# Optimization experiments

Measured on AMD Instinct MI355X. Metric: run time of the kernel, lower is better.

## Reference

```python
import jax, jax.numpy as jnp
import numpy as np
from jax import lax

DIM = 192
NUM_CLASSES = 4
D_INNER = 2 * DIM          # expand=2
D_STATE = 16
D_CONV = 4
DT_RANK = (DIM + 15) // 16  # ceil(192/16)=12
PATCH = 16


def _mamba_params(key, prefix):
    ks = jax.random.split(key, 9)
    s = lambda k, shape, scale: (jax.random.normal(k, shape, jnp.float32) * scale)
    p = {
        prefix + '_in_w':   s(ks[0], (2 * D_INNER, DIM), 0.02),
        prefix + '_conv_w': s(ks[1], (D_INNER, D_CONV), 0.1),
        prefix + '_conv_b': jnp.zeros((D_INNER,), jnp.float32),
        prefix + '_xproj_w': s(ks[2], (DT_RANK + 2 * D_STATE, D_INNER), 0.02),
        prefix + '_dt_w':   s(ks[3], (D_INNER, DT_RANK), 0.1),
        prefix + '_dt_b':   s(ks[4], (D_INNER,), 0.1),
        # A_log init: log(1..d_state) broadcast over d_inner (mamba default)
        prefix + '_A_log':  jnp.broadcast_to(jnp.log(jnp.arange(1, D_STATE + 1, dtype=jnp.float32)), (D_INNER, D_STATE)) + 0.0,
        prefix + '_D':      jnp.ones((D_INNER,), jnp.float32),
        prefix + '_out_w':  s(ks[5], (DIM, D_INNER), 0.02),
    }
    return p


def setup_inputs() -> dict:
    key = jax.random.key(0)
    ks = jax.random.split(key, 8)
    inp = {
        'x': jax.random.normal(ks[0], (32, 3, 384, 384), jnp.float32),
        'patch_w': jax.random.normal(ks[1], (DIM, 3, PATCH, PATCH), jnp.float32) * 0.02,
        'patch_b': jnp.zeros((DIM,), jnp.float32),
        'ln_g': jnp.ones((DIM,), jnp.float32),
        'ln_b': jnp.zeros((DIM,), jnp.float32),
        'fc_w': jax.random.normal(ks[2], (NUM_CLASSES, DIM), jnp.float32) * 0.02,
        'fc_b': jnp.zeros((NUM_CLASSES,), jnp.float32),
    }
    inp.update(_mamba_params(ks[3], 'f'))
    inp.update(_mamba_params(ks[4], 'b'))
    return inp


def _layernorm(x, g, b, eps=1e-5):
    mu = jnp.mean(x, -1, keepdims=True)
    var = jnp.mean(jnp.square(x - mu), -1, keepdims=True)
    return (x - mu) * lax.rsqrt(var + eps) * g + b


def _mamba(x, in_w, conv_w, conv_b, xproj_w, dt_w, dt_b, A_log, Dskip, out_w):
    # x: [B, L, DIM]
    Bn, L, _ = x.shape
    xz = x @ in_w.T                                    # [B, L, 2*di]
    xi, z = jnp.split(xz, 2, axis=-1)
    # causal depthwise conv1d, kernel D_CONV, left pad
    xp = jnp.pad(xi, ((0, 0), (D_CONV - 1, 0), (0, 0)))
    xc = conv_b + sum(xp[:, k:k + L, :] * conv_w[:, k] for k in range(D_CONV))
    xc = jax.nn.silu(xc)                               # [B, L, di]
    proj = xc @ xproj_w.T                              # [B, L, dtr+2*ds]
    dt, Bm, Cm = jnp.split(proj, [DT_RANK, DT_RANK + D_STATE], axis=-1)
    dt = jax.nn.softplus(dt @ dt_w.T + dt_b)           # [B, L, di]
    A = -jnp.exp(A_log)                                # [di, ds]

    def step(h, inp):
        dt_t, B_t, C_t, x_t = inp                      # [B,di],[B,ds],[B,ds],[B,di]
        dA = jnp.exp(dt_t[:, :, None] * A)             # [B, di, ds]
        h = dA * h + (dt_t * x_t)[:, :, None] * B_t[:, None, :]
        y = jnp.einsum('bds,bs->bd', h, C_t)
        return h, y

    h0 = jnp.zeros((Bn, D_INNER, D_STATE), x.dtype)
    xs = (dt.transpose(1, 0, 2), Bm.transpose(1, 0, 2),
          Cm.transpose(1, 0, 2), xc.transpose(1, 0, 2))
    _, ys = lax.scan(step, h0, xs)                     # [L, B, di]
    y = ys.transpose(1, 0, 2) + xc * Dskip
    y = y * jax.nn.silu(z)
    return y @ out_w.T                                 # [B, L, DIM]


def reference(x, patch_w, patch_b, ln_g, ln_b, fc_w, fc_b,
              f_in_w, f_conv_w, f_conv_b, f_xproj_w, f_dt_w, f_dt_b, f_A_log, f_D, f_out_w,
              b_in_w, b_conv_w, b_conv_b, b_xproj_w, b_dt_w, b_dt_b, b_A_log, b_D, b_out_w):
    Bn, C, H, W = x.shape
    Hp, Wp = H // PATCH, W // PATCH
    # patch embed: stride==kernel conv == reshape + einsum
    xr = x.reshape(Bn, C, Hp, PATCH, Wp, PATCH)
    tok = jnp.einsum('bchpwq,dcpq->bhwd', xr, patch_w) + patch_b
    tok = tok.reshape(Bn, Hp * Wp, DIM)                # [B, L, D]
    tok = _layernorm(tok, ln_g, ln_b)
    fwd = _mamba(tok, f_in_w, f_conv_w, f_conv_b, f_xproj_w, f_dt_w, f_dt_b, f_A_log, f_D, f_out_w)
    bwd = _mamba(tok[:, ::-1, :], b_in_w, b_conv_w, b_conv_b, b_xproj_w, b_dt_w, b_dt_b, b_A_log, b_D, b_out_w)
    out = fwd + bwd[:, ::-1, :]
    pooled = jnp.mean(out, axis=1)                     # adaptive avg pool to 1
    return pooled @ fc_w.T + fc_b                      # [B, num_classes]
```

## Files before the change

### kernel.cpp

```cpp
#include <hip/hip_runtime.h>
#include <hip/hip_bf16.h>

#define NC 32
#define CL 18

typedef __attribute__((ext_vector_type(8))) short short8;
typedef __attribute__((ext_vector_type(4))) float f32x4;
typedef __attribute__((ext_vector_type(2))) float f32x2;

__device__ __forceinline__ float sigm(float x){ return 1.0f/(1.0f+__expf(-x)); }

__device__ __forceinline__ ushort f2bf(float f){
  unsigned u = __float_as_uint(f);
  unsigned r = (u + 0x7fffu + ((u>>16)&1u)) >> 16;
  return (ushort)r;
}
__device__ __forceinline__ float bf2f(ushort h){ return __uint_as_float(((unsigned)h)<<16); }

__global__ __launch_bounds__(256) void k_prep_all(
    const float* __restrict__ patch_w, const float* __restrict__ f_in_w,
    const float* __restrict__ b_in_w,
    const float* __restrict__ f_xw, const float* __restrict__ b_xw,
    const float* __restrict__ f_cw, const float* __restrict__ b_cw,
    const float* __restrict__ f_al, const float* __restrict__ b_al,
    const float* __restrict__ fc_w, const float* __restrict__ f_ow,
    const float* __restrict__ b_ow,
    ushort* __restrict__ pw_h, ushort* __restrict__ pw_l,
    ushort* __restrict__ iw_h, ushort* __restrict__ iw_l,
    ushort* __restrict__ xw_h, ushort* __restrict__ xw_l,
    float* __restrict__ cwT, float* __restrict__ Abuf,
    float* __restrict__ A0fl, float* __restrict__ W2){
  const int bx = blockIdx.x, t = threadIdx.x;
  if (bx < 1728){
    int which = bx/576;
    int i = (bx - which*576)*256 + t;
    if (which==0){
      float f = patch_w[i];
      ushort hb = f2bf(f);
      pw_h[i]=hb; pw_l[i]=f2bf(f - bf2f(hb));
    } else {
      const float* src = (which==1) ? f_in_w : b_in_w;
      int dirofs = (which==1) ? 0 : 48;
      float f = src[i];
      int n = i/192, k = i%192;
      int nblk = n>>4, r = n&15, kblk = k>>5, kk = k&31;
      int lane = r + ((kk>>3)<<4), j = kk&7;
      size_t idx = ((size_t)((nblk+dirofs)*6 + kblk)*64 + lane)*8 + j;
      ushort hb = f2bf(f);
      iw_h[idx]=hb; iw_l[idx]=f2bf(f - bf2f(hb));
    }
  } else if (bx < 1872){
    int i = (bx-1728)*256 + t;
    int dir=i/(48*384), rem=i%(48*384), n=rem/384, k=rem%384;
    float v = (n<44) ? (dir?b_xw:f_xw)[n*384+k] : 0.f;
    ushort hb = f2bf(v);
    xw_h[i]=hb; xw_l[i]=f2bf(v - bf2f(hb));
  } else if (bx < 1884){
    int i = (bx-1872)*256 + t;
    int dir=i/1536, rem=i%1536, j=rem/384, k=rem%384;
    cwT[i] = (dir ? b_cw : f_cw)[k*4+j];
  } else if (bx < 1887){
    int i = (bx-1884)*256 + t;
    if (i < 768){
      int dir=i/384, di=i%384;
      const float* alp = (dir?b_al:f_al) + di*16;
      float A0 = -expf(alp[0]);
      bool fast = true;
      Abuf[(size_t)i*16] = A0;
      #pragma unroll
      for (int s=1;s<16;s++){
        float A = -expf(alp[s]);
        Abuf[(size_t)i*16+s] = A;
        fast = fast && (fabsf(A - (s+1)*A0) <= 1e-5f*(s+1)*fabsf(A0));
      }
      A0fl[i*2]=A0; A0fl[i*2+1]=fast?1.f:0.f;
    }
  } else {
    int i = (bx-1887)*256 + t;
    if (i < 768){
      int dir=i/384, di=i%384;
      const float* ow = dir ? b_ow : f_ow;
      float a0=0.f,a1=0.f,a2=0.f,a3=0.f;
      for (int d=0; d<192; ++d){
        float o = ow[d*384 + di];
        a0 += fc_w[0*192+d]*o; a1 += fc_w[1*192+d]*o;
        a2 += fc_w[2*192+d]*o; a3 += fc_w[3*192+d]*o;
      }
      W2[(0*2+dir)*384+di]=a0; W2[(1*2+dir)*384+di]=a1;
      W2[(2*2+dir)*384+di]=a2; W2[(3*2+dir)*384+di]=a3;
    }
  }
}

__global__ __launch_bounds__(1024) void k_patch(
    const float* __restrict__ x,
    const ushort* __restrict__ pw_h, const ushort* __restrict__ pw_l,
    const float* __restrict__ pb, const float* __restrict__ lng,
    const float* __restrict__ lnb,
    ushort* __restrict__ tokf_h, ushort* __restrict__ tokf_l,
    int b0, int Mc){
  __shared__ __align__(16) char sBmem[49152];
  __shared__ __align__(16) ushort sAh[64*64], sAl[64*64];
  __shared__ float sLN[4][64][2];
  ushort* sBh = (ushort*)sBmem;
  ushort* sBl = (ushort*)(sBmem + 24576);
  const int tid = threadIdx.x;
  const int m0 = blockIdx.x*64;
  const int lane = tid&63, w = tid>>6;
  const int wr = w>>2, wc = w&3;
  const int r = lane&15, g = lane>>4;
  f32x4 acc[3];
  #pragma unroll
  for (int i=0;i<3;i++) acc[i] = (f32x4){0.f,0.f,0.f,0.f};

  const int mA = tid>>4, remA = tid&15, ppA = remA>>2, qqA = remA&3;
  const int rmA = m0 + mA;
  const bool okA = (rmA < Mc);
  size_t baseA = 0;
  if (okA){
    int b = b0 + rmA/576, l = rmA%576, hp = l/24, wp = l%24;
    baseA = ((size_t)(b*3)*384 + hp*16 + ppA)*96 + wp*4 + qqA;
  }
  const int nB0 = tid>>3, k8B0 = tid&7;
  const bool okB1 = (tid < 512);
  const int fB1 = tid + 1024;
  const int nB1 = fB1>>3, k8B1 = fB1&7;
  const int byteA  = (mA*128 + ppA*32 + qqA*8) ^ ((mA&7)<<4);
  const int byteB0 = (nB0*128 + k8B0*16) ^ ((nB0&7)<<4);
  const int byteB1 = (nB1*128 + k8B1*16) ^ ((nB1&7)<<4);

  float4 vA = make_float4(0.f,0.f,0.f,0.f);
  uint4 vBh0 = {}, vBl0 = {}, vBh1 = {}, vBl1 = {};
  {
    if (okA) vA = reinterpret_cast<const float4*>(x)[baseA];
    size_t gi0 = (size_t)nB0*768 + k8B0*8;
    vBh0 = *reinterpret_cast<const uint4*>(pw_h + gi0);
    vBl0 = *reinterpret_cast<const uint4*>(pw_l + gi0);
    if (okB1){
      size_t gi1 = (size_t)nB1*768 + k8B1*8;
      vBh1 = *reinterpret_cast<const uint4*>(pw_h + gi1);
      vBl1 = *reinterpret_cast<const uint4*>(pw_l + gi1);
    }
  }

  for (int s=0;s<12;s++){
    {
      ushort4 hv, lv;
      hv.x=f2bf(vA.x); lv.x=f2bf(vA.x-bf2f(hv.x));
      hv.y=f2bf(vA.y); lv.y=f2bf(vA.y-bf2f(hv.y));
      hv.z=f2bf(vA.z); lv.z=f2bf(vA.z-bf2f(hv.z));
      hv.w=f2bf(vA.w); lv.w=f2bf(vA.w-bf2f(hv.w));
      *reinterpret_cast<ushort4*>((char*)sAh + byteA) = hv;
      *reinterpret_cast<ushort4*>((char*)sAl + byteA) = lv;
      *reinterpret_cast<uint4*>((char*)sBh + byteB0) = vBh0;
      *reinterpret_cast<uint4*>((char*)sBl + byteB0) = vBl0;
      if (okB1){
        *reinterpret_cast<uint4*>((char*)sBh + byteB1) = vBh1;
        *reinterpret_cast<uint4*>((char*)sBl + byteB1) = vBl1;
      }
    }
    __syncthreads();
    if (s < 11){
      int s1 = s+1, c1 = s1>>2, p01 = (s1&3)*4;
      if (okA) vA = reinterpret_cast<const float4*>(x)[baseA + ((size_t)c1*384 + p01)*96];
      size_t gi0 = (size_t)nB0*768 + (size_t)s1*64 + k8B0*8;
      vBh0 = *reinterpret_cast<const uint4*>(pw_h + gi0);
      vBl0 = *reinterpret_cast<const uint4*>(pw_l + gi0);
      if (okB1){
        size_t gi1 = (size_t)nB1*768 + (size_t)s1*64 + k8B1*8;
        vBh1 = *reinterpret_cast<const uint4*>(pw_h + gi1);
        vBl1 = *reinterpret_cast<const uint4*>(pw_l + gi1);
      }
    }
    #pragma unroll
    for (int kk=0;kk<2;kk++){
      int arow = wr*16 + r;
      int abyte = (arow*128 + kk*64 + g*16) ^ ((arow&7)<<4);
      short8 ah = *reinterpret_cast<const short8*>((char*)sAh + abyte);
      short8 al = *reinterpret_cast<const short8*>((char*)sAl + abyte);
      #pragma unroll
      for (int nfl=0; nfl<3; nfl++){
        int brow = (wc*3+nfl)*16 + r;
        int bbyte = (brow*128 + kk*64 + g*16) ^ ((brow&7)<<4);
        short8 bh = *reinterpret_cast<const short8*>((char*)sBh + bbyte);
        short8 bll = *reinterpret_cast<const short8*>((char*)sBl + bbyte);
        acc[nfl] = __builtin_amdgcn_mfma_f32_16x16x32_bf16(ah, bh, acc[nfl], 0,0,0);
        acc[nfl] = __builtin_amdgcn_mfma_f32_16x16x32_bf16(ah, bll, acc[nfl], 0,0,0);
        acc[nfl] = __builtin_amdgcn_mfma_f32_16x16x32_bf16(al, bh, acc[nfl], 0,0,0);
      }
    }
    __syncthreads();
  }
  float pbv[3], gv[3], bv[3];
  #pragma unroll
  for (int nfl=0;nfl<3;nfl++){
    int col = (wc*3+nfl)*16 + r;
    pbv[nfl]=pb[col]; gv[nfl]=lng[col]; bv[nfl]=lnb[col];
  }
  #pragma unroll
  for (int nfl=0;nfl<3;nfl++)
    #pragma unroll
    for (int q=0;q<4;q++) acc[nfl][q] += pbv[nfl];
  float sum[4]={0,0,0,0}, sq[4]={0,0,0,0};
  #pragma unroll
  for (int nfl=0;nfl<3;nfl++)
    #pragma unroll
    for (int q=0;q<4;q++){ float v=acc[nfl][q]; sum[q]+=v; sq[q]+=v*v; }
  #pragma unroll
  for (int off=1; off<16; off<<=1){
    #pragma unroll
    for (int q=0;q<4;q++){
      sum[q]+=__shfl_xor(sum[q],off);
      sq[q] +=__shfl_xor(sq[q],off);
    }
  }
  if (r==0){
    #pragma unroll
    for (int q=0;q<4;q++){
      int row = wr*16 + g*4 + q;
      sLN[wc][row][0]=sum[q]; sLN[wc][row][1]=sq[q];
    }
  }
  __syncthreads();
  float* sT = (float*)sBmem;
  #pragma unroll
  for (int q=0;q<4;q++){
    int rl = wr*16 + g*4 + q;
    float stot = sLN[0][rl][0]+sLN[1][rl][0]+sLN[2][rl][0]+sLN[3][rl][0];
    float qtot = sLN[0][rl][1]+sLN[1][rl][1]+sLN[2][rl][1]+sLN[3][rl][1];
    float mu = stot*(1.f/192.f);
    float var = qtot*(1.f/192.f) - mu*mu;
    float rs = rsqrtf(var + 1e-5f);
    #pragma unroll
    for (int nfl=0;nfl<3;nfl++)
      sT[rl*192 + (wc*3+nfl)*16 + r] = (acc[nfl][q]-mu)*rs*gv[nfl] + bv[nfl];
  }
  __syncthreads();
  const int mB = m0>>4;
  #pragma unroll
  for (int i=0;i<2;i++){
    int fl = tid + 1024*i;
    if (fl < 1536){
      int mb = fl/384, rem = fl-mb*384, kb = rem>>6, ln = rem&63;
      int rr = ln&15, gq = ln>>4;
      const float* sp = sT + (mb*16+rr)*192 + kb*32 + gq*8;
      short8 hv, lv;
      #pragma unroll
      for (int j=0;j<8;j++){
        float v = sp[j];
        ushort hb = f2bf(v);
        hv[j] = (short)hb;
        lv[j] = (short)f2bf(v - bf2f(hb));
      }
      size_t o = ((size_t)((mB+mb)*6 + kb)*64 + ln)*8;
      *reinterpret_cast<short8*>(tokf_h + o) = hv;
      *reinterpret_cast<short8*>(tokf_l + o) = lv;
    }
  }
}

__global__ __launch_bounds__(1024) void k_inproj(
    const ushort* __restrict__ tokf_h, const ushort* __restrict__ tokf_l,
    const ushort* __restrict__ iw_h, const ushort* __restrict__ iw_l,
    float* __restrict__ xib, ushort* __restrict__ zb, int Bc, int Mc){
  __shared__ __align__(16) char sMem[65536];
  ushort* sAh = (ushort*)sMem;
  ushort* sAl = (ushort*)(sMem + 16384);
  ushort* sBh = (ushort*)(sMem + 32768);
  ushort* sBl = (ushort*)(sMem + 49152);
  const int tid = threadIdx.x;
  const int lane = tid&63, w = tid>>6;
  const int wr = w>>2, wc = w&3;
  const int r = lane&15, g = lane>>4;
  const int m0 = blockIdx.x*128;
  const int mb0 = blockIdx.x*8;
  const int nb0 = blockIdx.y*8;
  const int n0d = (blockIdx.y%6)*128;
  const bool dir1 = (blockIdx.y >= 6);
  const bool isZ = ((blockIdx.y%6) >= 3);

  f32x4 acc[2][2];
  #pragma unroll
  for (int a=0;a<2;a++)
    #pragma unroll
    for (int b=0;b<2;b++) acc[a][b] = (f32x4){0.f,0.f,0.f,0.f};

  for (int s=0;s<3;s++){
    {
      const int f = w;
      const int mf = f>>1, kk = f&1;
      const size_t ga = ((size_t)((mb0+mf)*6 + 2*s+kk)*64 + lane)*8;
      const size_t gb = ((size_t)((nb0+mf)*6 + 2*s+kk)*64 + lane)*8;
      const int so = f*512 + lane*8;
      *reinterpret_cast<short8*>(sAh+so) = *reinterpret_cast<const short8*>(tokf_h+ga);
      *reinterpret_cast<short8*>(sBh+so) = *reinterpret_cast<const short8*>(iw_h+gb);
      if (!isZ){
        *reinterpret_cast<short8*>(sAl+so) = *reinterpret_cast<const short8*>(tokf_l+ga);
        *reinterpret_cast<short8*>(sBl+so) = *reinterpret_cast<const short8*>(iw_l+gb);
      }
    }
    __syncthreads();
    #pragma unroll
    for (int kk=0;kk<2;kk++){
      short8 ah[2], al[2];
      #pragma unroll
      for (int mf=0;mf<2;mf++){
        const int fo = ((wr*2+mf)*2+kk)*512 + lane*8;
        ah[mf] = *reinterpret_cast<const short8*>(sAh+fo);
        if (!isZ) al[mf] = *reinterpret_cast<const short8*>(sAl+fo);
      }
      #pragma unroll
      for (int nf=0;nf<2;nf++){
        const int fo = ((wc*2+nf)*2+kk)*512 + lane*8;
        short8 bh = *reinterpret_cast<const short8*>(sBh+fo);
        if (isZ){
          #pragma unroll
          for (int mf=0;mf<2;mf++)
            acc[mf][nf] = __builtin_amdgcn_mfma_f32_16x16x32_bf16(ah[mf], bh, acc[mf][nf], 0,0,0);
        } else {
          short8 bl = *reinterpret_cast<const short8*>(sBl+fo);
          #pragma unroll
          for (int mf=0;mf<2;mf++){
            acc[mf][nf] = __builtin_amdgcn_mfma_f32_16x16x32_bf16(ah[mf], bh, acc[mf][nf], 0,0,0);
            acc[mf][nf] = __builtin_amdgcn_mfma_f32_16x16x32_bf16(ah[mf], bl, acc[mf][nf], 0,0,0);
            acc[mf][nf] = __builtin_amdgcn_mfma_f32_16x16x32_bf16(al[mf], bh, acc[mf][nf], 0,0,0);
          }
        }
      }
    }
    __syncthreads();
  }

  float* sT = reinterpret_cast<float*>(sMem);
  const int h_of_w = wr>>1;
  #pragma unroll
  for (int h=0; h<2; h++){
    if (h==1) __syncthreads();
    if (h_of_w == h){
      #pragma unroll
      for (int mf=0;mf<2;mf++)
        #pragma unroll
        for (int nf=0;nf<2;nf++)
          #pragma unroll
          for (int q=0;q<4;q++){
            int rl = (wr&1)*32 + mf*16 + g*4 + q;
            int c  = wc*32 + nf*16 + r;
            sT[rl*132 + c] = acc[mf][nf][q];
          }
    }
    __syncthreads();
    {
      const int rl = tid>>4, cg = tid&15;
      const int rm = m0 + h*64 + rl;
      if (rm < Mc){
        size_t row;
        if (dir1){
          int bl = rm/576, l = rm - bl*576;
          row = (size_t)(Bc + bl)*576 + (575-l);
        } else {
          row = (size_t)rm;
        }
        const float* sp = sT + rl*132 + cg*8;
        if (!isZ){
          *reinterpret_cast<f32x4*>(xib + row*384 + n0d + cg*8)     = *reinterpret_cast<const f32x4*>(sp);
          *reinterpret_cast<f32x4*>(xib + row*384 + n0d + cg*8 + 4) = *reinterpret_cast<const f32x4*>(sp+4);
        } else {
          short8 hv;
          #pragma unroll
          for (int j=0;j<8;j++){
            float v = sp[j];
            v = v*sigm(v);
            hv[j] = (short)f2bf(v);
          }
          *reinterpret_cast<short8*>(zb + row*384 + (n0d-384) + cg*8) = hv;
        }
      }
    }
  }
}

__global__ __launch_bounds__(256) void k_convx(
    const float* __restrict__ xib, const float* __restrict__ cwT,
    const float* __restrict__ f_cb, const float* __restrict__ b_cb,
    const ushort* __restrict__ xw_h, const ushort* __restrict__ xw_l,
    float* __restrict__ proj, ushort* __restrict__ xcb, int Bc){
  __shared__ __align__(16) float sRaw[67*64];
  __shared__ __align__(16) ushort sAh[64*64], sAl[64*64];
  __shared__ __align__(16) ushort sBh[48*64], sBl[48*64];
  const int dir = blockIdx.z, blk = blockIdx.y, l0 = blockIdx.x*64;
  const int tid = threadIdx.x, lane = tid&63, w = tid>>6;
  const int r = lane&15, g = lane>>4;
  const size_t seq = ((size_t)dir*Bc + blk)*576;
  const float* cwTd = cwT + dir*1536;
  const float* cbp  = dir?b_cb:f_cb;
  const ushort* bhp = xw_h + dir*48*384;
  const ushort* blp = xw_l + dir*48*384;
  f32x4 acc[3];
  #pragma unroll
  for (int i=0;i<3;i++) acc[i] = (f32x4){0.f,0.f,0.f,0.f};

  for (int kc=0; kc<6; ++kc){
    #pragma unroll
    for (int i=0;i<5;i++){
      int f = tid + i*256;
      if (f < 67*16){
        int rr = f>>4, kq = f&15;
        int l = l0 + rr - 3;
        float4 v = make_float4(0.f,0.f,0.f,0.f);
        if (l >= 0) v = *reinterpret_cast<const float4*>(xib + (seq+l)*384 + kc*64 + kq*4);
        int kqs = kq ^ (rr&15);
        *reinterpret_cast<float4*>(sRaw + rr*64 + kqs*4) = v;
      }
    }
    __syncthreads();
    #pragma unroll
    for (int i=0;i<4;i++){
      int f = tid + i*256;
      int m = f>>4, kq = f&15;
      float4 a = reinterpret_cast<const float4*>(cbp)[kc*16 + kq];
      #pragma unroll
      for (int j=0;j<4;j++){
        int rr = m + j;
        float4 rv = *reinterpret_cast<const float4*>(sRaw + rr*64 + (kq ^ (rr&15))*4);
        float4 cv = reinterpret_cast<const float4*>(cwTd)[j*96 + kc*16 + kq];
        a.x += cv.x*rv.x; a.y += cv.y*rv.y; a.z += cv.z*rv.z; a.w += cv.w*rv.w;
      }
      a.x = a.x*sigm(a.x); a.y = a.y*sigm(a.y); a.z = a.z*sigm(a.z); a.w = a.w*sigm(a.w);
      ushort4 hv, lv;
      hv.x=f2bf(a.x); lv.x=f2bf(a.x-bf2f(hv.x));
      hv.y=f2bf(a.y); lv.y=f2bf(a.y-bf2f(hv.y));
      hv.z=f2bf(a.z); lv.z=f2bf(a.z-bf2f(hv.z));
      hv.w=f2bf(a.w); lv.w=f2bf(a.w-bf2f(hv.w));
      *reinterpret_cast<ushort4*>(xcb + (seq + l0 + m)*384 + kc*64 + kq*4) = hv;
      int byte = (m*128 + kq*8) ^ ((m&7)<<4);
      *reinterpret_cast<ushort4*>((char*)sAh + byte) = hv;
      *reinterpret_cast<ushort4*>((char*)sAl + byte) = lv;
    }
    #pragma unroll
    for (int i=0;i<2;i++){
      int f = tid + i*256;
      if (f < 384){
        int n = f>>3, k8 = f&7;
        size_t gi = (size_t)n*384 + kc*64 + k8*8;
        uint4 vh = *reinterpret_cast<const uint4*>(bhp + gi);
        uint4 vl = *reinterpret_cast<const uint4*>(blp + gi);
        int byte = (n*128 + k8*16) ^ ((n&7)<<4);
        *reinterpret_cast<uint4*>((char*)sBh + byte) = vh;
        *reinterpret_cast<uint4*>((char*)sBl + byte) = vl;
      }
    }
    __syncthreads();
    #pragma unroll
    for (int kk=0;kk<2;kk++){
      int arow = w*16 + r;
      int abyte = (arow*128 + kk*64 + g*16) ^ ((arow&7)<<4);
      short8 ah = *reinterpret_cast<const short8*>((char*)sAh + abyte);
      short8 al = *reinterpret_cast<const short8*>((char*)sAl + abyte);
      #pragma unroll
      for (int nf=0;nf<3;nf++){
        int brow = nf*16 + r;
        int bbyte = (brow*128 + kk*64 + g*16) ^ ((brow&7)<<4);
        short8 bh = *reinterpret_cast<const short8*>((char*)sBh + bbyte);
        short8 bll = *reinterpret_cast<const short8*>((char*)sBl + bbyte);
        acc[nf] = __builtin_amdgcn_mfma_f32_16x16x32_bf16(ah, bh, acc[nf], 0,0,0);
        acc[nf] = __builtin_amdgcn_mfma_f32_16x16x32_bf16(ah, bll, acc[nf], 0,0,0);
        acc[nf] = __builtin_amdgcn_mfma_f32_16x16x32_bf16(al, bh, acc[nf], 0,0,0);
      }
    }
    __syncthreads();
  }
  #pragma unroll
  for (int nf=0;nf<3;nf++){
    int col = nf*16 + r;
    if (col < 44){
      #pragma unroll
      for (int q=0;q<4;q++){
        int l = l0 + w*16 + g*4 + q;
        proj[(seq+l)*44 + col] = acc[nf][q];
      }
    }
  }
}

__global__ __launch_bounds__(256) void k_scan_p1(
    const ushort* __restrict__ zb, const ushort* __restrict__ xcb,
    const float* __restrict__ proj,
    const float* __restrict__ f_dtw, const float* __restrict__ b_dtw,
    const float* __restrict__ f_dtb, const float* __restrict__ b_dtb,
    const float* __restrict__ A0fl, const float* __restrict__ Abuf,
    const float* __restrict__ f_D,  const float* __restrict__ b_D,
    const float* __restrict__ W2, float* __restrict__ dtend,
    float* __restrict__ hbuf, float* __restrict__ Gbuf,
    float* __restrict__ part, int b0, int Bc){
  const int dir=blockIdx.z, bl=blockIdx.y;
  const int gg=blockIdx.x>>3, cq=blockIdx.x&7;
  const int wv=threadIdx.x>>6, lane=threadIdx.x&63;
  const int c = cq*4 + wv;
  const int di0 = gg*128 + lane*2;
  const size_t seq = ((size_t)dir*Bc + bl)*576;
  const float* dtwp = (dir?b_dtw:f_dtw) + (size_t)di0*12;
  f32x2 dtw2[12];
  {
    const float4* dp = reinterpret_cast<const float4*>(dtwp);
    #pragma unroll
    for (int i=0;i<3;i++){
      float4 fa = dp[i], fb = dp[i+3];
      dtw2[4*i+0] = (f32x2){fa.x, fb.x};
      dtw2[4*i+1] = (f32x2){fa.y, fb.y};
      dtw2[4*i+2] = (f32x2){fa.z, fb.z};
      dtw2[4*i+3] = (f32x2){fa.w, fb.w};
    }
  }
  float2 dtb2 = *reinterpret_cast<const float2*>((dir?b_dtb:f_dtb)+di0);
  float4 af = *reinterpret_cast<const float4*>(A0fl + ((size_t)dir*384+di0)*2);
  const float A0a = af.x, A0b = af.z;
  const bool fast = (af.y != 0.f) && (af.w != 0.f);
  const float* Abp = Abuf + ((size_t)dir*384+di0)*16;
  float2 Dv2 = *reinterpret_cast<const float2*>((dir?b_D:f_D)+di0);
  float2 w2c2[4];
  #pragma unroll
  for (int ch=0;ch<4;ch++)
    w2c2[ch] = *reinterpret_cast<const float2*>(W2 + (ch*2+dir)*384 + di0);
  f32x2 h2a[8], h2b[8], P2a[8], P2b[8], G2a[8], G2b[8];
  #pragma unroll
  for (int p=0;p<8;p++){
    h2a[p]=(f32x2){0.f,0.f}; h2b[p]=(f32x2){0.f,0.f};
    P2a[p]=(f32x2){1.f,1.f}; P2b[p]=(f32x2){1.f,1.f};
    G2a[p]=(f32x2){0.f,0.f}; G2b[p]=(f32x2){0.f,0.f};
  }
  float Sa=0.f, Sb=0.f, cuma=0.f, cumb=0.f;
  const int l0 = c*CL;
  const int pbase = (int)((seq + (size_t)l0)*44);
  const ushort* xcp = xcb + di0;
  const ushort* zbp2 = zb + di0;
  for (int j=0;j<CL;j++){
    const size_t row = seq + l0 + j;
    const int po = __builtin_amdgcn_readfirstlane(pbase + j*44);
    const float4* pr4 = reinterpret_cast<const float4*>(proj + po);
    float4 t0=pr4[0], t1=pr4[1], t2=pr4[2];
    f32x2 dtin2 = (f32x2){dtb2.x, dtb2.y};
    dtin2 += (f32x2){t0.x,t0.x}*dtw2[0]; dtin2 += (f32x2){t0.y,t0.y}*dtw2[1];
    dtin2 += (f32x2){t0.z,t0.z}*dtw2[2]; dtin2 += (f32x2){t0.w,t0.w}*dtw2[3];
    dtin2 += (f32x2){t1.x,t1.x}*dtw2[4]; dtin2 += (f32x2){t1.y,t1.y}*dtw2[5];
    dtin2 += (f32x2){t1.z,t1.z}*dtw2[6]; dtin2 += (f32x2){t1.w,t1.w}*dtw2[7];
    dtin2 += (f32x2){t2.x,t2.x}*dtw2[8]; dtin2 += (f32x2){t2.y,t2.y}*dtw2[9];
    dtin2 += (f32x2){t2.z,t2.z}*dtw2[10]; dtin2 += (f32x2){t2.w,t2.w}*dtw2[11];
    float dta = (dtin2[0] > 20.f) ? dtin2[0] : __logf(1.f + __expf(dtin2[0]));
    float dtb_ = (dtin2[1] > 20.f) ? dtin2[1] : __logf(1.f + __expf(dtin2[1]));
    cuma += dta; cumb += dtb_;
    uint xu = *reinterpret_cast<const uint*>(xcp + row*384);
    uint zu = *reinterpret_cast<const uint*>(zbp2 + row*384);
    float xca = bf2f((ushort)(xu&0xffffu)), xcbv = bf2f((ushort)(xu>>16));
    float zsa = bf2f((ushort)(zu&0xffffu)), zsb = bf2f((ushort)(zu>>16));
    float ua = dta*xca, ub = dtb_*xcbv;
    f32x2 u2a = {ua,ua}, u2b = {ub,ub};
    f32x2 zsa2 = {zsa,zsa}, zsb2 = {zsb,zsb};
    f32x2 dA2a[8], dA2b[8];
    if (fast){
      float e1a=__expf(dta*A0a);
      float e2a=e1a*e1a;
      f32x2 e2va={e2a,e2a};
      dA2a[0]=(f32x2){e1a,e2a};
      #pragma unroll
      for (int p=1;p<8;p++) dA2a[p]=dA2a[p-1]*e2va;
      float e1b=__expf(dtb_*A0b);
      float e2b=e1b*e1b;
      f32x2 e2vb={e2b,e2b};
      dA2b[0]=(f32x2){e1b,e2b};
      #pragma unroll
      for (int p=1;p<8;p++) dA2b[p]=dA2b[p-1]*e2vb;
    } else {
      #pragma unroll
      for (int p=0;p<8;p++){
        dA2a[p]=(f32x2){__expf(dta*Abp[2*p]), __expf(dta*Abp[2*p+1])};
        dA2b[p]=(f32x2){__expf(dtb_*Abp[16+2*p]), __expf(dtb_*Abp[16+2*p+1])};
      }
    }
    f32x2 yaa={0.f,0.f}, yba={0.f,0.f}, yab={0.f,0.f}, ybb={0.f,0.f};
    #pragma unroll
    for (int i=0;i<4;i++){
      float4 tb4=pr4[3+i], tc4=pr4[7+i];
      f32x2 B0={tb4.x,tb4.y}, B1={tb4.z,tb4.w};
      f32x2 C0={tc4.x,tc4.y}, C1={tc4.z,tc4.w};
      h2a[2*i]   = dA2a[2*i]*h2a[2*i]     + u2a*B0;
      h2a[2*i+1] = dA2a[2*i+1]*h2a[2*i+1] + u2a*B1;
      yaa += h2a[2*i]*C0;
      yba += h2a[2*i+1]*C1;
      h2b[2*i]   = dA2b[2*i]*h2b[2*i]     + u2b*B0;
      h2b[2*i+1] = dA2b[2*i+1]*h2b[2*i+1] + u2b*B1;
      yab += h2b[2*i]*C0;
      ybb += h2b[2*i+1]*C1;
      P2a[2*i]   *= dA2a[2*i];   P2a[2*i+1] *= dA2a[2*i+1];
      P2b[2*i]   *= dA2b[2*i];   P2b[2*i+1] *= dA2b[2*i+1];
      f32x2 Cz0a = C0*zsa2, Cz1a = C1*zsa2;
      f32x2 Cz0b = C0*zsb2, Cz1b = C1*zsb2;
      G2a[2*i]   += Cz0a*P2a[2*i];
      G2a[2*i+1] += Cz1a*P2a[2*i+1];
      G2b[2*i]   += Cz0b*P2b[2*i];
      G2b[2*i+1] += Cz1b*P2b[2*i+1];
    }
    Sa += ((yaa[0]+yaa[1])+(yba[0]+yba[1]) + xca*Dv2.x)*zsa;
    Sb += ((yab[0]+yab[1])+(ybb[0]+ybb[1]) + xcbv*Dv2.y)*zsb;
  }
  *reinterpret_cast<float2*>(dtend + ((((size_t)dir*Bc + bl)*NC + c)*384 + di0))
      = make_float2(cuma, cumb);
  size_t hb = ((((size_t)c*2+dir)*Bc + bl)*3 + gg)*2048;
  #pragma unroll
  for (int s=0;s<16;s++){
    *reinterpret_cast<float2*>(hbuf + hb + s*128 + lane*2)
        = make_float2(h2a[s>>1][s&1], h2b[s>>1][s&1]);
    *reinterpret_cast<float2*>(Gbuf + hb + s*128 + lane*2)
        = make_float2(G2a[s>>1][s&1], G2b[s>>1][s&1]);
  }
  float p0 = Sa*w2c2[0].x + Sb*w2c2[0].y;
  float p1v= Sa*w2c2[1].x + Sb*w2c2[1].y;
  float p2v= Sa*w2c2[2].x + Sb*w2c2[2].y;
  float p3v= Sa*w2c2[3].x + Sb*w2c2[3].y;
  #pragma unroll
  for (int off=32; off>0; off>>=1){
    p0 += __shfl_xor(p0, off); p1v += __shfl_xor(p1v, off);
    p2v += __shfl_xor(p2v, off); p3v += __shfl_xor(p3v, off);
  }
  if (lane==0){
    float* dst = part + ((((size_t)dir*32 + (b0+bl))*3 + gg)*32 + c)*4;
    dst[0]=p0; dst[1]=p1v; dst[2]=p2v; dst[3]=p3v;
  }
}

__global__ __launch_bounds__(256) void k_combine(
    const float* __restrict__ dtend, const float* __restrict__ hbuf,
    const float* __restrict__ Gbuf,
    const float* __restrict__ A0fl, const float* __restrict__ Abuf,
    const float* __restrict__ W2, float* __restrict__ part2,
    int b0, int Bc){
  const int gg=blockIdx.x, bl=blockIdx.y, dir=blockIdx.z;
  const int wv=threadIdx.x>>6, lane=threadIdx.x&63;
  const int di0=gg*128+lane*2;
  float4 af = *reinterpret_cast<const float4*>(A0fl + ((size_t)dir*384+di0)*2);
  const bool fast = (af.y != 0.f) && (af.w != 0.f);
  const float* Abp = Abuf + ((size_t)dir*384+di0)*16;
  float Aa[4], Ab[4];
  #pragma unroll
  for (int si=0;si<4;si++){
    int s = wv*4+si;
    Aa[si] = fast ? af.x*(float)(s+1) : Abp[s];
    Ab[si] = fast ? af.z*(float)(s+1) : Abp[16+s];
  }
  float2 w2c2[4];
  #pragma unroll
  for (int ch=0;ch<4;ch++)
    w2c2[ch] = *reinterpret_cast<const float2*>(W2 + (ch*2+dir)*384 + di0);
  float2 cur[4];
  size_t hx0 = ((((size_t)(0*2+dir)*Bc+bl)*3+gg)*2048) + (wv*4)*128 + lane*2;
  #pragma unroll
  for (int si=0;si<4;si++) cur[si]=*reinterpret_cast<const float2*>(hbuf + hx0 + si*128);
  for (int c=1;c<NC;c++){
    size_t hx=((((size_t)c*2+dir)*Bc+bl)*3+gg)*2048 + (wv*4)*128 + lane*2;
    float ta=0.f, tb=0.f;
    float2 tmp[4];
    #pragma unroll
    for (int si=0;si<4;si++){
      tmp[si]=*reinterpret_cast<const float2*>(hbuf+hx+si*128);
      float2 Gv = *reinterpret_cast<const float2*>(Gbuf+hx+si*128);
      ta += cur[si].x*Gv.x;
      tb += cur[si].y*Gv.y;
    }
    float p0 = ta*w2c2[0].x + tb*w2c2[0].y;
    float p1v= ta*w2c2[1].x + tb*w2c2[1].y;
    float p2v= ta*w2c2[2].x + tb*w2c2[2].y;
    float p3v= ta*w2c2[3].x + tb*w2c2[3].y;
    #pragma unroll
    for (int off=32; off>0; off>>=1){
      p0 += __shfl_xor(p0, off); p1v += __shfl_xor(p1v, off);
      p2v += __shfl_xor(p2v, off); p3v += __shfl_xor(p3v, off);
    }
    if (lane==0){
      float* dst = part2 + (((((size_t)(dir*32 + (b0+bl))*3 + gg)*4 + wv)*32) + c)*4;
      dst[0]=p0; dst[1]=p1v; dst[2]=p2v; dst[3]=p3v;
    }
    if (c<NC-1){
      float2 Sdt = *reinterpret_cast<const float2*>(dtend + ((((size_t)dir*Bc+bl)*NC + c)*384 + di0));
      #pragma unroll
      for (int si=0;si<4;si++){
        cur[si].x = __expf(Aa[si]*Sdt.x)*cur[si].x + tmp[si].x;
        cur[si].y = __expf(Ab[si]*Sdt.y)*cur[si].y + tmp[si].y;
      }
    }
  }
}

__global__ __launch_bounds__(256) void k_final(const float* __restrict__ part,
                                               const float* __restrict__ part2,
                                               const float* __restrict__ fc_b,
                                               float* __restrict__ out){
  const int b = blockIdx.x;
  const int ch = threadIdx.x>>6, lane = threadIdx.x&63;
  float s = 0.f;
  for (int i = lane; i < 192; i += 64){
    int c = i & 31;
    int dg = i >> 5;
    int dir = dg >= 3 ? 1 : 0;
    int gg = dg - dir*3;
    s += part[((((size_t)dir*32 + b)*3 + gg)*32 + c)*4 + ch];
  }
  for (int i = lane; i < 768; i += 64){
    int c = i & 31;
    if (c == 0) continue;
    int t = i >> 5;
    int dir = t >= 12 ? 1 : 0;
    int rem = t - dir*12;
    int gg = rem >> 2, wv = rem & 3;
    s += part2[(((((size_t)(dir*32 + b)*3 + gg)*4 + wv)*32) + c)*4 + ch];
  }
  #pragma unroll
  for (int off=32; off>0; off>>=1) s += __shfl_xor(s, off);
  if (lane==0) out[b*4+ch] = fc_b[ch] + s*(1.0f/576.0f);
}

extern "C" void kernel_launch(void* const* d_in, const int* in_sizes, int n_in,
                              void* d_out, int out_size, void* d_ws, size_t ws_size,
                              hipStream_t stream){
  const float* x       = (const float*)d_in[0];
  const float* patch_w = (const float*)d_in[1];
  const float* patch_b = (const float*)d_in[2];
  const float* ln_g    = (const float*)d_in[3];
  const float* ln_b    = (const float*)d_in[4];
  const float* fc_w    = (const float*)d_in[5];
  const float* fc_b    = (const float*)d_in[6];
  const float* f_in_w  = (const float*)d_in[7];
  const float* f_cw    = (const float*)d_in[8];
  const float* f_cb    = (const float*)d_in[9];
  const float* f_xw    = (const float*)d_in[10];
  const float* f_dtw   = (const float*)d_in[11];
  const float* f_dtb   = (const float*)d_in[12];
  const float* f_al    = (const float*)d_in[13];
  const float* f_D     = (const float*)d_in[14];
  const float* f_ow    = (const float*)d_in[15];
  const float* b_in_w  = (const float*)d_in[16];
  const float* b_cw    = (const float*)d_in[17];
  const float* b_cb    = (const float*)d_in[18];
  const float* b_xw    = (const float*)d_in[19];
  const float* b_dtw   = (const float*)d_in[20];
  const float* b_dtb   = (const float*)d_in[21];
  const float* b_al    = (const float*)d_in[22];
  const float* b_D     = (const float*)d_in[23];
  const float* b_ow    = (const float*)d_in[24];
  float* out = (float*)d_out;
  float* ws  = (float*)d_ws;

  float* W2    = ws;
  float* part  = W2 + 3072;
  float* part2 = part + 24576;
  ushort* pw_h = (ushort*)(part2 + 98304);
  ushort* pw_l = pw_h + 147456;
  ushort* iw_h = pw_l + 147456;
  ushort* iw_l = iw_h + 294912;
  ushort* xw_h = iw_l + 294912;
  ushort* xw_l = xw_h + 36864;
  float* cwT   = (float*)(xw_l + 36864);
  float* Abuf  = cwT + 3072;
  float* A0fl  = Abuf + 12288;
  float* base  = A0fl + 1536;

  const size_t FIXED = 622080ull;
  const size_t perB  = 1806336ull;
  int Bc = 32;
  while (Bc > 1 && (FIXED + (size_t)Bc*perB)*4ull > ws_size) Bc >>= 1;

  ushort* tokf_h = (ushort*)base;
  ushort* tokf_l = tokf_h + (size_t)Bc*110592ull;
  float* prj  = base;
  float* xib  = base + (size_t)Bc*110592ull;
  ushort* zbp = (ushort*)(xib + (size_t)Bc*442368ull);
  ushort* xcb = zbp + (size_t)Bc*442368ull;
  float* dtnd = (float*)(xcb + (size_t)Bc*442368ull);
  float* hbf  = dtnd + (size_t)Bc*24576ull;
  float* Gbf  = hbf + (size_t)Bc*393216ull;

  k_prep_all<<<dim3(1890),dim3(256),0,stream>>>(patch_w, f_in_w, b_in_w,
                                                f_xw, b_xw, f_cw, b_cw,
                                                f_al, b_al, fc_w, f_ow, b_ow,
                                                pw_h, pw_l, iw_h, iw_l,
                                                xw_h, xw_l, cwT, Abuf, A0fl, W2);

  for (int b0=0; b0<32; b0+=Bc){
    const int Mc = Bc*576;
    k_patch<<<dim3((Mc+63)/64),dim3(1024),0,stream>>>(x, pw_h, pw_l, patch_b,
                                                      ln_g, ln_b, tokf_h, tokf_l, b0, Mc);
    k_inproj<<<dim3((Mc+127)/128,12),dim3(1024),0,stream>>>(tokf_h, tokf_l, iw_h, iw_l,
                                                            xib, zbp, Bc, Mc);
    k_convx<<<dim3(9,Bc,2),dim3(256),0,stream>>>(xib, cwT, f_cb, b_cb,
                                                 xw_h, xw_l, prj, xcb, Bc);
    k_scan_p1<<<dim3(24,Bc,2),dim3(256),0,stream>>>(zbp, xcb, prj,
                                                    f_dtw,b_dtw, f_dtb,b_dtb,
                                                    A0fl, Abuf, f_D,b_D,
                                                    W2, dtnd, hbf, Gbf, part, b0, Bc);
    k_combine<<<dim3(3,Bc,2),dim3(256),0,stream>>>(dtnd, hbf, Gbf, A0fl, Abuf,
                                                   W2, part2, b0, Bc);
  }
  k_final<<<dim3(32),dim3(256),0,stream>>>(part, part2, fc_b, out);
}
```

Before: 240.3 us.

## Replace carried G-accumulator chunk correction with a second scan pass over chunks

The chunked scan no longer keeps the P and G accumulators that encoded how the incoming chunk state contributes to the output. The combine kernel now writes each chunk's incoming state back into hbuf. A new k_scan_p2 kernel replays the decay and C-projection from that state, using saved dt values, to compute the missing output contribution. This removes register pressure and Gbuf traffic from the first pass. In exchange it adds a kernel launch, dt stores, and a second read of proj, z and dt.

New measurement: 229.4 us. -4.5%, faster.

```diff
diff --git a/kernel.cpp b/kernel.cpp
--- a/kernel.cpp
+++ b/kernel.cpp
@@ -490,7 +490,7 @@
     const float* __restrict__ A0fl, const float* __restrict__ Abuf,
     const float* __restrict__ f_D,  const float* __restrict__ b_D,
     const float* __restrict__ W2, float* __restrict__ dtend,
-    float* __restrict__ hbuf, float* __restrict__ Gbuf,
+    float* __restrict__ hbuf, float* __restrict__ dtsav,
     float* __restrict__ part, int b0, int Bc){
   const int dir=blockIdx.z, bl=blockIdx.y;
   const int gg=blockIdx.x>>3, cq=blockIdx.x&7;
@@ -521,13 +521,9 @@
   #pragma unroll
   for (int ch=0;ch<4;ch++)
     w2c2[ch] = *reinterpret_cast<const float2*>(W2 + (ch*2+dir)*384 + di0);
-  f32x2 h2a[8], h2b[8], P2a[8], P2b[8], G2a[8], G2b[8];
-  #pragma unroll
-  for (int p=0;p<8;p++){
-    h2a[p]=(f32x2){0.f,0.f}; h2b[p]=(f32x2){0.f,0.f};
-    P2a[p]=(f32x2){1.f,1.f}; P2b[p]=(f32x2){1.f,1.f};
-    G2a[p]=(f32x2){0.f,0.f}; G2b[p]=(f32x2){0.f,0.f};
-  }
+  f32x2 h2a[8], h2b[8];
+  #pragma unroll
+  for (int p=0;p<8;p++){ h2a[p]=(f32x2){0.f,0.f}; h2b[p]=(f32x2){0.f,0.f}; }
   float Sa=0.f, Sb=0.f, cuma=0.f, cumb=0.f;
   const int l0 = c*CL;
   const int pbase = (int)((seq + (size_t)l0)*44);
@@ -548,13 +544,14 @@
     float dta = (dtin2[0] > 20.f) ? dtin2[0] : __logf(1.f + __expf(dtin2[0]));
     float dtb_ = (dtin2[1] > 20.f) ? dtin2[1] : __logf(1.f + __expf(dtin2[1]));
     cuma += dta; cumb += dtb_;
+    if (c != 0)
+      *reinterpret_cast<float2*>(dtsav + row*384 + di0) = make_float2(dta, dtb_);
     uint xu = *reinterpret_cast<const uint*>(xcp + row*384);
     uint zu = *reinterpret_cast<const uint*>(zbp2 + row*384);
     float xca = bf2f((ushort)(xu&0xffffu)), xcbv = bf2f((ushort)(xu>>16));
     float zsa = bf2f((ushort)(zu&0xffffu)), zsb = bf2f((ushort)(zu>>16));
     float ua = dta*xca, ub = dtb_*xcbv;
     f32x2 u2a = {ua,ua}, u2b = {ub,ub};
-    f32x2 zsa2 = {zsa,zsa}, zsb2 = {zsb,zsb};
     f32x2 dA2a[8], dA2b[8];
     if (fast){
       float e1a=__expf(dta*A0a);
@@ -590,14 +587,6 @@
       h2b[2*i+1] = dA2b[2*i+1]*h2b[2*i+1] + u2b*B1;
       yab += h2b[2*i]*C0;
       ybb += h2b[2*i+1]*C1;
-      P2a[2*i]   *= dA2a[2*i];   P2a[2*i+1] *= dA2a[2*i+1];
-      P2b[2*i]   *= dA2b[2*i];   P2b[2*i+1] *= dA2b[2*i+1];
-      f32x2 Cz0a = C0*zsa2, Cz1a = C1*zsa2;
-      f32x2 Cz0b = C0*zsb2, Cz1b = C1*zsb2;
-      G2a[2*i]   += Cz0a*P2a[2*i];
-      G2a[2*i+1] += Cz1a*P2a[2*i+1];
-      G2b[2*i]   += Cz0b*P2b[2*i];
-      G2b[2*i+1] += Cz1b*P2b[2*i+1];
     }
     Sa += ((yaa[0]+yaa[1])+(yba[0]+yba[1]) + xca*Dv2.x)*zsa;
     Sb += ((yab[0]+yab[1])+(ybb[0]+ybb[1]) + xcbv*Dv2.y)*zsb;
@@ -606,12 +595,9 @@
       = make_float2(cuma, cumb);
   size_t hb = ((((size_t)c*2+dir)*Bc + bl)*3 + gg)*2048;
   #pragma unroll
-  for (int s=0;s<16;s++){
+  for (int s=0;s<16;s++)
     *reinterpret_cast<float2*>(hbuf + hb + s*128 + lane*2)
         = make_float2(h2a[s>>1][s&1], h2b[s>>1][s&1]);
-    *reinterpret_cast<float2*>(Gbuf + hb + s*128 + lane*2)
-        = make_float2(G2a[s>>1][s&1], G2b[s>>1][s&1]);
-  }
   float p0 = Sa*w2c2[0].x + Sb*w2c2[0].y;
   float p1v= Sa*w2c2[1].x + Sb*w2c2[1].y;
   float p2v= Sa*w2c2[2].x + Sb*w2c2[2].y;
@@ -622,17 +608,14 @@
     p2v += __shfl_xor(p2v, off); p3v += __shfl_xor(p3v, off);
   }
   if (lane==0){
-    float* dst = part + ((((size_t)dir*32 + (b0+bl))*3 + gg)*32 + c)*4;
+    float* dst = part + ((((size_t)dir*32 + (b0+bl))*3 + gg)*64 + c)*4;
     dst[0]=p0; dst[1]=p1v; dst[2]=p2v; dst[3]=p3v;
   }
 }
 
 __global__ __launch_bounds__(256) void k_combine(
-    const float* __restrict__ dtend, const float* __restrict__ hbuf,
-    const float* __restrict__ Gbuf,
-    const float* __restrict__ A0fl, const float* __restrict__ Abuf,
-    const float* __restrict__ W2, float* __restrict__ part2,
-    int b0, int Bc){
+    const float* __restrict__ dtend, float* __restrict__ hbuf,
+    const float* __restrict__ A0fl, const float* __restrict__ Abuf, int Bc){
   const int gg=blockIdx.x, bl=blockIdx.y, dir=blockIdx.z;
   const int wv=threadIdx.x>>6, lane=threadIdx.x&63;
   const int di0=gg*128+lane*2;
@@ -646,37 +629,17 @@
     Aa[si] = fast ? af.x*(float)(s+1) : Abp[s];
     Ab[si] = fast ? af.z*(float)(s+1) : Abp[16+s];
   }
-  float2 w2c2[4];
-  #pragma unroll
-  for (int ch=0;ch<4;ch++)
-    w2c2[ch] = *reinterpret_cast<const float2*>(W2 + (ch*2+dir)*384 + di0);
   float2 cur[4];
   size_t hx0 = ((((size_t)(0*2+dir)*Bc+bl)*3+gg)*2048) + (wv*4)*128 + lane*2;
   #pragma unroll
-  for (int si=0;si<4;si++) cur[si]=*reinterpret_cast<const float2*>(hbuf + hx0 + si*128);
+  for (int si=0;si<4;si++) cur[si]=*reinterpret_cast<float2*>(hbuf + hx0 + si*128);
   for (int c=1;c<NC;c++){
     size_t hx=((((size_t)c*2+dir)*Bc+bl)*3+gg)*2048 + (wv*4)*128 + lane*2;
-    float ta=0.f, tb=0.f;
     float2 tmp[4];
     #pragma unroll
     for (int si=0;si<4;si++){
-      tmp[si]=*reinterpret_cast<const float2*>(hbuf+hx+si*128);
-      float2 Gv = *reinterpret_cast<const float2*>(Gbuf+hx+si*128);
-      ta += cur[si].x*Gv.x;
-      tb += cur[si].y*Gv.y;
-    }
-    float p0 = ta*w2c2[0].x + tb*w2c2[0].y;
-    float p1v= ta*w2c2[1].x + tb*w2c2[1].y;
-    float p2v= ta*w2c2[2].x + tb*w2c2[2].y;
-    float p3v= ta*w2c2[3].x + tb*w2c2[3].y;
-    #pragma unroll
-    for (int off=32; off>0; off>>=1){
-      p0 += __shfl_xor(p0, off); p1v += __shfl_xor(p1v, off);
-      p2v += __shfl_xor(p2v, off); p3v += __shfl_xor(p3v, off);
-    }
-    if (lane==0){
-      float* dst = part2 + (((((size_t)(dir*32 + (b0+bl))*3 + gg)*4 + wv)*32) + c)*4;
-      dst[0]=p0; dst[1]=p1v; dst[2]=p2v; dst[3]=p3v;
+      tmp[si]=*reinterpret_cast<float2*>(hbuf+hx+si*128);
+      *reinterpret_cast<float2*>(hbuf+hx+si*128)=cur[si];
     }
     if (c<NC-1){
       float2 Sdt = *reinterpret_cast<const float2*>(dtend + ((((size_t)dir*Bc+bl)*NC + c)*384 + di0));
@@ -689,28 +652,111 @@
   }
 }
 
+__global__ __launch_bounds__(256) void k_scan_p2(
+    const ushort* __restrict__ zb, const float* __restrict__ proj,
+    const float* __restrict__ hbuf, const float* __restrict__ dtsav,
+    const float* __restrict__ A0fl, const float* __restrict__ Abuf,
+    const float* __restrict__ W2, float* __restrict__ part, int b0, int Bc){
+  const int dir=blockIdx.z, bl=blockIdx.y;
+  const int gg=blockIdx.x>>3, cq=blockIdx.x&7;
+  const int wv=threadIdx.x>>6, lane=threadIdx.x&63;
+  const int c = cq*4 + wv + 1;
+  const int di0 = gg*128 + lane*2;
+  const size_t seq = ((size_t)dir*Bc + bl)*576;
+  if (c >= NC) return;
+  float4 af = *reinterpret_cast<const float4*>(A0fl + ((size_t)dir*384+di0)*2);
+  const float A0a = af.x, A0b = af.z;
+  const bool fast = (af.y != 0.f) && (af.w != 0.f);
+  const float* Abp = Abuf + ((size_t)dir*384+di0)*16;
+  float2 w2c2[4];
+  #pragma unroll
+  for (int ch=0;ch<4;ch++)
+    w2c2[ch] = *reinterpret_cast<const float2*>(W2 + (ch*2+dir)*384 + di0);
+  f32x2 hh2a[8], hh2b[8];
+  size_t hb=((((size_t)c*2+dir)*Bc+bl)*3+gg)*2048;
+  #pragma unroll
+  for (int s=0;s<16;s++){
+    float2 v = *reinterpret_cast<const float2*>(hbuf + hb + s*128 + lane*2);
+    hh2a[s>>1][s&1]=v.x; hh2b[s>>1][s&1]=v.y;
+  }
+  float Sa=0.f, Sb=0.f;
+  const int l0 = c*CL;
+  const int pbase = (int)((seq + (size_t)l0)*44);
+  const ushort* zbp2 = zb + di0;
+  for (int j=0;j<CL;j++){
+    const size_t row = seq + l0 + j;
+    const int po = __builtin_amdgcn_readfirstlane(pbase + j*44);
+    const float4* pr4 = reinterpret_cast<const float4*>(proj + po);
+    float2 dtv = *reinterpret_cast<const float2*>(dtsav + row*384 + di0);
+    float dta = dtv.x, dtb_ = dtv.y;
+    uint zu = *reinterpret_cast<const uint*>(zbp2 + row*384);
+    float zsa = bf2f((ushort)(zu&0xffffu)), zsb = bf2f((ushort)(zu>>16));
+    f32x2 dA2a[8], dA2b[8];
+    if (fast){
+      float e1a=__expf(dta*A0a);
+      float e2a=e1a*e1a;
+      f32x2 e2va={e2a,e2a};
+      dA2a[0]=(f32x2){e1a,e2a};
+      #pragma unroll
+      for (int p=1;p<8;p++) dA2a[p]=dA2a[p-1]*e2va;
+      float e1b=__expf(dtb_*A0b);
+      float e2b=e1b*e1b;
+      f32x2 e2vb={e2b,e2b};
+      dA2b[0]=(f32x2){e1b,e2b};
+      #pragma unroll
+      for (int p=1;p<8;p++) dA2b[p]=dA2b[p-1]*e2vb;
+    } else {
+      #pragma unroll
+      for (int p=0;p<8;p++){
+        dA2a[p]=(f32x2){__expf(dta*Abp[2*p]), __expf(dta*Abp[2*p+1])};
+        dA2b[p]=(f32x2){__expf(dtb_*Abp[16+2*p]), __expf(dtb_*Abp[16+2*p+1])};
+      }
+    }
+    f32x2 yaa={0.f,0.f}, yba={0.f,0.f}, yab={0.f,0.f}, ybb={0.f,0.f};
+    #pragma unroll
+    for (int i=0;i<4;i++){
+      float4 tc4 = pr4[7+i];
+      f32x2 C0={tc4.x,tc4.y}, C1={tc4.z,tc4.w};
+      hh2a[2*i]   = hh2a[2*i]*dA2a[2*i];
+      hh2a[2*i+1] = hh2a[2*i+1]*dA2a[2*i+1];
+      yaa += hh2a[2*i]*C0;
+      yba += hh2a[2*i+1]*C1;
+      hh2b[2*i]   = hh2b[2*i]*dA2b[2*i];
+      hh2b[2*i+1] = hh2b[2*i+1]*dA2b[2*i+1];
+      yab += hh2b[2*i]*C0;
+      ybb += hh2b[2*i+1]*C1;
+    }
+    Sa += ((yaa[0]+yaa[1])+(yba[0]+yba[1]))*zsa;
+    Sb += ((yab[0]+yab[1])+(ybb[0]+ybb[1]))*zsb;
+  }
+  float p0 = Sa*w2c2[0].x + Sb*w2c2[0].y;
+  float p1v= Sa*w2c2[1].x + Sb*w2c2[1].y;
+  float p2v= Sa*w2c2[2].x + Sb*w2c2[2].y;
+  float p3v= Sa*w2c2[3].x + Sb*w2c2[3].y;
+  #pragma unroll
+  for (int off=32; off>0; off>>=1){
+    p0 += __shfl_xor(p0, off); p1v += __shfl_xor(p1v, off);
+    p2v += __shfl_xor(p2v, off); p3v += __shfl_xor(p3v, off);
+  }
+  if (lane==0){
+    float* dst = part + ((((size_t)dir*32 + (b0+bl))*3 + gg)*64 + 32 + c)*4;
+    dst[0]=p0; dst[1]=p1v; dst[2]=p2v; dst[3]=p3v;
+  }
+}
+
 __global__ __launch_bounds__(256) void k_final(const float* __restrict__ part,
-                                               const float* __restrict__ part2,
                                                const float* __restrict__ fc_b,
                                                float* __restrict__ out){
   const int b = blockIdx.x;
   const int ch = threadIdx.x>>6, lane = threadIdx.x&63;
   float s = 0.f;
-  for (int i = lane; i < 192; i += 64){
-    int c = i & 31;
-    int dg = i >> 5;
+  for (int i = lane; i < 384; i += 64){
+    int c = i & 63;
+    if (c == 32) continue;
+    int dg = i >> 6;
     int dir = dg >= 3 ? 1 : 0;
-    int gg = dg - dir*3;
-    s += part[((((size_t)dir*32 + b)*3 + gg)*32 + c)*4 + ch];
-  }
-  for (int i = lane; i < 768; i += 64){
-    int c = i & 31;
-    if (c == 0) continue;
-    int t = i >> 5;
-    int dir = t >= 12 ? 1 : 0;
-    int rem = t - dir*12;
-    int gg = rem >> 2, wv = rem & 3;
-    s += part2[(((((size_t)(dir*32 + b)*3 + gg)*4 + wv)*32) + c)*4 + ch];
+    int g = dg - dir*3;
+    s += part[((((size_t)dir*32 + b)*3 + g)*64 + c)*4 + ch];
   }
   #pragma unroll
   for (int off=32; off>0; off>>=1) s += __shfl_xor(s, off);
@@ -750,8 +796,7 @@
 
   float* W2    = ws;
   float* part  = W2 + 3072;
-  float* part2 = part + 24576;
-  ushort* pw_h = (ushort*)(part2 + 98304);
+  ushort* pw_h = (ushort*)(part + 98304);
   ushort* pw_l = pw_h + 147456;
   ushort* iw_h = pw_l + 147456;
   ushort* iw_l = iw_h + 294912;
@@ -762,8 +807,8 @@
   float* A0fl  = Abuf + 12288;
   float* base  = A0fl + 1536;
 
-  const size_t FIXED = 622080ull;
-  const size_t perB  = 1806336ull;
+  const size_t FIXED = 597504ull;
+  const size_t perB  = 1413120ull;
   int Bc = 32;
   while (Bc > 1 && (FIXED + (size_t)Bc*perB)*4ull > ws_size) Bc >>= 1;
 
@@ -771,11 +816,11 @@
   ushort* tokf_l = tokf_h + (size_t)Bc*110592ull;
   float* prj  = base;
   float* xib  = base + (size_t)Bc*110592ull;
+  float* dtsav = xib;
   ushort* zbp = (ushort*)(xib + (size_t)Bc*442368ull);
   ushort* xcb = zbp + (size_t)Bc*442368ull;
   float* dtnd = (float*)(xcb + (size_t)Bc*442368ull);
   float* hbf  = dtnd + (size_t)Bc*24576ull;
-  float* Gbf  = hbf + (size_t)Bc*393216ull;
 
   k_prep_all<<<dim3(1890),dim3(256),0,stream>>>(patch_w, f_in_w, b_in_w,
                                                 f_xw, b_xw, f_cw, b_cw,
@@ -794,9 +839,10 @@
     k_scan_p1<<<dim3(24,Bc,2),dim3(256),0,stream>>>(zbp, xcb, prj,
                                                     f_dtw,b_dtw, f_dtb,b_dtb,
                                                     A0fl, Abuf, f_D,b_D,
-                                                    W2, dtnd, hbf, Gbf, part, b0, Bc);
-    k_combine<<<dim3(3,Bc,2),dim3(256),0,stream>>>(dtnd, hbf, Gbf, A0fl, Abuf,
-                                                   W2, part2, b0, Bc);
-  }
-  k_final<<<dim3(32),dim3(256),0,stream>>>(part, part2, fc_b, out);
-}
+                                                    W2, dtnd, hbf, dtsav, part, b0, Bc);
+    k_combine<<<dim3(3,Bc,2),dim3(256),0,stream>>>(dtnd, hbf, A0fl, Abuf, Bc);
+    k_scan_p2<<<dim3(24,Bc,2),dim3(256),0,stream>>>(zbp, prj, hbf, dtsav,
+                                                    A0fl, Abuf, W2, part, b0, Bc);
+  }
+  k_final<<<dim3(32),dim3(256),0,stream>>>(part, fc_b, out);
+}
```
